# Kernel tuning notes

Measured on AMD Instinct MI355X. Metric: run time of the kernel, lower is better.

Reference implementation:

```python
import jax, jax.numpy as jnp
import numpy as np
import math

B, S, D = 8, 1024, 1024
NH, NKV, HD = 16, 8, 64
BLK_NUM, BLK_SIZE = 128, 8

def apply_rope(x, cos, sin):
    # x: (B,S,H,HD); cos/sin: (S, HD//2)
    x1 = x[..., 0::2]
    x2 = x[..., 1::2]
    c = cos[None, :, None, :]
    s = sin[None, :, None, :]
    r1 = x1 * c - x2 * s
    r2 = x1 * s + x2 * c
    out = jnp.stack([r1, r2], axis=-1).reshape(x.shape)
    return out

def setup_inputs() -> dict:
    key = jax.random.key(0)
    ks = jax.random.split(key, 7)
    x = jax.random.normal(ks[0], (B, S, D), dtype=jnp.float32)
    scale = 1.0 / math.sqrt(D)
    wq = jax.random.normal(ks[1], (D, NH * HD), dtype=jnp.float32) * scale
    wk = jax.random.normal(ks[2], (D, NKV * HD), dtype=jnp.float32) * scale
    wv = jax.random.normal(ks[3], (D, NKV * HD), dtype=jnp.float32) * scale
    wo = jax.random.normal(ks[4], (NH * HD, D), dtype=jnp.float32) * scale
    pos = jnp.arange(S, dtype=jnp.float32)
    inv_freq = 1.0 / (10000.0 ** (jnp.arange(0, HD, 2, dtype=jnp.float32) / HD))
    ang = pos[:, None] * inv_freq[None, :]
    freqs_cis_cos = jnp.cos(ang)
    freqs_cis_sin = jnp.sin(ang)
    return {"x": x, "wq": wq, "wk": wk, "wv": wv, "wo": wo,
            "freqs_cis_cos": freqs_cis_cos, "freqs_cis_sin": freqs_cis_sin,
            "start_pos": 0}

def reference(x, wq, wk, wv, wo, freqs_cis_cos, freqs_cis_sin, start_pos):
    q = (x @ wq).reshape(B, S, NH, HD)
    k = (x @ wk).reshape(B, S, NKV, HD)
    v = (x @ wv).reshape(B, S, NKV, HD)
    q = apply_rope(q, freqs_cis_cos, freqs_cis_sin)
    k = apply_rope(k, freqs_cis_cos, freqs_cis_sin)
    # GQA: repeat kv heads
    rep = NH // NKV
    k = jnp.repeat(k, rep, axis=2)  # (B,S,NH,HD)
    v = jnp.repeat(v, rep, axis=2)
    # block-causal mask: q in block i attends to kv blocks j <= i
    blk_id = jnp.arange(S) // BLK_SIZE
    mask = blk_id[:, None] >= blk_id[None, :]  # (S,S)
    scores = jnp.einsum('bqhd,bkhd->bhqk', q, k) / math.sqrt(HD)
    scores = jnp.where(mask[None, None], scores, -jnp.inf)
    attn = jax.nn.softmax(scores, axis=-1)
    out = jnp.einsum('bhqk,bkhd->bqhd', attn, v).reshape(B, S, NH * HD)
    return out @ wo
```

## Files before the change

### kernel.cpp

```cpp
#include <hip/hip_runtime.h>
#include <cstdint>
#include <math.h>

#define B_   8
#define S_   1024
#define D_   1024
#define NH_  16
#define NKV_ 8
#define HD_  64
#define M_   (B_*S_)

using bf16   = __bf16;
using bf16x4 = __attribute__((ext_vector_type(4))) __bf16;
using bf16x8 = __attribute__((ext_vector_type(8))) __bf16;
using f32x4  = __attribute__((ext_vector_type(4))) float;

__device__ __forceinline__ void gll16(const bf16* g, const bf16* l) {
    __builtin_amdgcn_global_load_lds(
        (const __attribute__((address_space(1))) unsigned int*)(uintptr_t)g,
        (__attribute__((address_space(3))) unsigned int*)(uintptr_t)l,
        16, 0, 0);
}

__device__ __forceinline__ void dsr128(bf16x8& d, const bf16* p) {
    asm volatile("ds_read_b128 %0, %1" : "=v"(d) : "v"((unsigned)(uintptr_t)p));
}
__device__ __forceinline__ void lgkm0() {
    asm volatile("s_waitcnt lgkmcnt(0)" ::: "memory");
    __builtin_amdgcn_sched_barrier(0);
}
__device__ __forceinline__ void vm_wait0()  { asm volatile("s_waitcnt vmcnt(0)"  ::: "memory"); }
__device__ __forceinline__ void vm_wait4()  { asm volatile("s_waitcnt vmcnt(4)"  ::: "memory"); }
__device__ __forceinline__ void vm_wait6()  { asm volatile("s_waitcnt vmcnt(6)"  ::: "memory"); }
__device__ __forceinline__ void vm_wait8()  { asm volatile("s_waitcnt vmcnt(8)"  ::: "memory"); }
__device__ __forceinline__ void bar()       { __builtin_amdgcn_s_barrier(); asm volatile("" ::: "memory"); }

__global__ void k_prep1(const float* __restrict__ x,
                        const float* __restrict__ wq, const float* __restrict__ wk,
                        const float* __restrict__ wv, const float* __restrict__ wo,
                        bf16* __restrict__ xb, bf16* __restrict__ wqkvT, bf16* __restrict__ woT) {
    __shared__ float tile[64 * 65];
    int bid = blockIdx.x;
    int t = threadIdx.x;
    if (bid < 8192) {
        int i = bid * 256 + t;
        float4 v = ((const float4*)x)[i];
        bf16x4 o = { (bf16)v.x, (bf16)v.y, (bf16)v.z, (bf16)v.w };
        ((bf16x4*)xb)[i] = o;
        return;
    }
    int b2 = bid - 8192;
    int bx = b2 % 48, by = b2 / 48;
    const int R = 1024;
    const float* in; bf16* out; int C, xo;
    if (bx < 16)      { in = wq; out = wqkvT;               C = 1024; xo = bx; }
    else if (bx < 24) { in = wk; out = wqkvT + 1024 * 1024; C = 512;  xo = bx - 16; }
    else if (bx < 32) { in = wv; out = wqkvT + 1536 * 1024; C = 512;  xo = bx - 24; }
    else              { in = wo; out = woT;                 C = 1024; xo = bx - 32; }
    int r0 = by * 64, c0 = xo * 64;
    #pragma unroll
    for (int it = 0; it < 16; ++it) {
        int idx = it * 256 + t;
        int r = idx >> 6, c = idx & 63;
        tile[r * 65 + c] = in[(size_t)(r0 + r) * C + c0 + c];
    }
    __syncthreads();
    #pragma unroll
    for (int it = 0; it < 16; ++it) {
        int idx = it * 256 + t;
        int c = idx >> 6, r = idx & 63;
        out[(size_t)(c0 + c) * R + r0 + r] = (bf16)tile[r * 65 + c];
    }
}

template <typename OutT, int NFR>
__global__ __launch_bounds__(256, 1) void k_gemmW(const bf16* __restrict__ A,
                                                  const bf16* __restrict__ Bt,
                                                  OutT* __restrict__ C, int M, int N, int K) {
    constexpr int BN = NFR * 32;
    __shared__ __align__(16) bf16 aL3[3 * 256 * 32];
    __shared__ __align__(16) bf16 bL3[3 * BN * 32];
    const int t    = threadIdx.x;
    const int lane = t & 63;
    const int w    = t >> 6;
    const int quad = lane >> 4;
    const int l16  = lane & 15;
    const int wr   = w >> 1;
    const int wc   = w & 1;

    int bid = blockIdx.y * gridDim.x + blockIdx.x;
    int cpx = (gridDim.x * gridDim.y) >> 3;
    int sw  = (bid & 7) * cpx + (bid >> 3);
    int bx  = sw % gridDim.x, by = sw / gridDim.x;
    const int m0 = by * 256;
    const int n0 = bx * BN;

    f32x4 acc[8][NFR] = {};

    auto stage = [&](int kb, int sb) {
        const int k0 = kb << 5;
        #pragma unroll
        for (int it = 0; it < 4; ++it) {
            int u = it * 256 + t;
            int r = u >> 2, c = u & 3;
            int cg = c ^ ((r & 3) ^ ((r >> 2) & 3));
            gll16(A + (size_t)(m0 + r) * K + k0 + cg * 8, aL3 + sb * (256 * 32) + u * 8);
        }
        #pragma unroll
        for (int it = 0; it < BN / 64; ++it) {
            int u = it * 256 + t;
            int r = u >> 2, c = u & 3;
            int cg = c ^ ((r & 3) ^ ((r >> 2) & 3));
            gll16(Bt + (size_t)(n0 + r) * K + k0 + cg * 8, bL3 + sb * (BN * 32) + u * 8);
        }
    };

    const int NT = K >> 5;

    stage(0, 0);
    stage(1, 1);

    int cur = 0;
    for (int T = 0; T < NT; ++T) {
        if (T + 1 < NT) { if constexpr (NFR == 8) vm_wait8(); else vm_wait6(); }
        else vm_wait0();
        bar();

        const bf16* aT = aL3 + cur * (256 * 32);
        const bf16* bT = bL3 + cur * (BN * 32);
        bf16x8 af[8], bf[NFR];
        #pragma unroll
        for (int mi = 0; mi < 8; ++mi) {
            int row = wr * 128 + mi * 16 + l16;
            int ch  = quad ^ ((row & 3) ^ ((row >> 2) & 3));
            af[mi] = *(const bf16x8*)&aT[row * 32 + ch * 8];
        }
        #pragma unroll
        for (int ni = 0; ni < NFR; ++ni) {
            int row = wc * (NFR * 16) + ni * 16 + l16;
            int ch  = quad ^ ((row & 3) ^ ((row >> 2) & 3));
            bf[ni] = *(const bf16x8*)&bT[row * 32 + ch * 8];
        }

        int stg = cur + 2; if (stg >= 3) stg -= 3;
        if (T + 2 < NT) stage(T + 2, stg);

        #pragma unroll
        for (int mi = 0; mi < 8; ++mi)
            #pragma unroll
            for (int ni = 0; ni < NFR; ++ni)
                acc[mi][ni] = __builtin_amdgcn_mfma_f32_16x16x32_bf16(af[mi], bf[ni], acc[mi][ni], 0, 0, 0);

        cur = (cur == 2) ? 0 : cur + 1;
    }

    #pragma unroll
    for (int mi = 0; mi < 8; ++mi)
        #pragma unroll
        for (int ni = 0; ni < NFR; ++ni)
            #pragma unroll
            for (int r = 0; r < 4; ++r) {
                int row = m0 + wr * 128 + mi * 16 + quad * 4 + r;
                int col = n0 + wc * (NFR * 16) + ni * 16 + l16;
                C[(size_t)row * N + col] = (OutT)acc[mi][ni][r];
            }
}

__global__ void k_prep2(const bf16* __restrict__ qkv, const float* __restrict__ cosg,
                        const float* __restrict__ sing, bf16* __restrict__ qd,
                        bf16* __restrict__ kd, bf16* __restrict__ vt) {
    __shared__ __align__(16) bf16 tile[64 * 72];
    int bid = blockIdx.x;
    int t = threadIdx.x;
    if (bid < 8192) {
        if (t < 192) {
            int token = bid;
            int b = token >> 10, s = token & 1023;
            int hh = t >> 3, i8 = t & 7;
            float4 c4 = *(const float4*)&cosg[s * 32 + i8 * 4];
            float4 s4 = *(const float4*)&sing[s * 32 + i8 * 4];
            int srcBase, dstBase;
            bf16* dst;
            float sf;
            if (hh < 16) {
                srcBase = token * 2048 + hh * 64;
                dstBase = ((b * NH_ + hh) * S_ + s) * 64;
                dst = qd;
                sf = 0.180336879f;
            } else {
                int h = hh - 16;
                srcBase = token * 2048 + 1024 + h * 64;
                dstBase = ((b * NKV_ + h) * S_ + s) * 64;
                dst = kd;
                sf = 1.0f;
            }
            bf16x8 v = *(const bf16x8*)&qkv[srcBase + i8 * 8];
            const float cc[4] = { c4.x, c4.y, c4.z, c4.w };
            const float ss[4] = { s4.x, s4.y, s4.z, s4.w };
            bf16x8 o;
            #pragma unroll
            for (int j = 0; j < 4; ++j) {
                float e  = (float)v[2 * j];
                float od = (float)v[2 * j + 1];
                o[2 * j]     = (bf16)(sf * (e * cc[j] - od * ss[j]));
                o[2 * j + 1] = (bf16)(sf * (e * ss[j] + od * cc[j]));
            }
            *(bf16x8*)&dst[dstBase + i8 * 8] = o;
        }
        return;
    }
    int b2 = bid - 8192;
    int st = b2 & 15;
    int h  = (b2 >> 4) & 7;
    int b  = b2 >> 7;
    int s0 = st * 64;
    #pragma unroll
    for (int it = 0; it < 2; ++it) {
        int ci = it * 256 + t;
        int r = ci >> 3, c = ci & 7;
        *(uint4*)&tile[r * 72 + c * 8] =
            *(const uint4*)&qkv[(size_t)(b * S_ + s0 + r) * 2048 + 1536 + h * 64 + c * 8];
    }
    __syncthreads();
    #pragma unroll
    for (int it = 0; it < 2; ++it) {
        int ci = it * 256 + t;
        int d = ci >> 3, sc = ci & 7;
        int g = sc >> 2, q4 = sc & 3;
        bf16x8 v;
        #pragma unroll
        for (int j = 0; j < 8; ++j) {
            int s_ext = g * 32 + q4 * 4 + (j & 3) + 16 * (j >> 2);
            v[j] = tile[s_ext * 72 + d];
        }
        *(bf16x8*)&vt[(size_t)((b * NKV_ + h) * 64 + d) * S_ + s0 + sc * 8] = v;
    }
}

__global__ __launch_bounds__(256, 4) void k_attn(const bf16* __restrict__ q, const bf16* __restrict__ k,
                                                 const bf16* __restrict__ vt, bf16* __restrict__ out) {
    __shared__ __align__(16) bf16 kt[2 * 64 * 64];
    __shared__ __align__(16) bf16 vtt[2 * 64 * 64];
    int bid = blockIdx.x;
    int qt = 15 - (bid >> 7);
    int combo = bid & 127;
    int b = combo >> 4, h = combo & 15;
    int hkv = h >> 1;
    int t = threadIdx.x;
    int w = t >> 6, lane = t & 63, quad = lane >> 4, l16 = lane & 15;

    const bf16* qh = q + (size_t)(b * NH_ + h) * S_ * 64;
    int qw = qt * 64 + w * 16;
    const bf16* qb = qh + (size_t)(qw + l16) * 64;
    bf16x8 qf0 = *(const bf16x8*)(qb + quad * 8);
    bf16x8 qf1 = *(const bf16x8*)(qb + 32 + quad * 8);

    const bf16* kg = k  + (size_t)(b * NKV_ + hkv) * S_ * 64;
    const bf16* vg = vt + (size_t)(b * NKV_ + hkv) * 64 * S_;

    const int sr0 = t >> 3;
    const int cs  = t & 7;

    auto stage = [&](int u, int buf) {
        int k0 = u * 64;
        #pragma unroll
        for (int it = 0; it < 2; ++it) {
            int r  = sr0 + it * 32;
            int cg = cs ^ (r & 7);
            int ci = it * 256 + t;
            gll16(kg + (size_t)(k0 + r) * 64 + cg * 8, kt  + buf * 4096 + ci * 8);
            gll16(vg + (size_t)r * S_ + k0 + cg * 8,   vtt + buf * 4096 + ci * 8);
        }
    };

    const bf16 one = (bf16)1.0f;
    const bf16x8 vones = { one, one, one, one, one, one, one, one };

    f32x4 o[4] = {};
    f32x4 ol = {};
    const int klim = ((qw + l16) & ~7) + 8;

    auto unit = [&](const bf16* ktb, const bf16* vtb, int k0, bool diag) {
        bf16x8 af[8];
        #pragma unroll
        for (int kk = 0; kk < 2; ++kk)
            #pragma unroll
            for (int f = 0; f < 4; ++f) {
                int row = f * 16 + l16;
                int ch  = (kk * 4 + quad) ^ (row & 7);
                dsr128(af[kk * 4 + f], &ktb[row * 64 + ch * 8]);
            }
        lgkm0();
        f32x4 sc[4] = {};
        __builtin_amdgcn_s_setprio(1);
        #pragma unroll
        for (int kk = 0; kk < 2; ++kk)
            #pragma unroll
            for (int f = 0; f < 4; ++f)
                sc[f] = __builtin_amdgcn_mfma_f32_16x16x32_bf16(af[kk * 4 + f], kk ? qf1 : qf0, sc[f], 0, 0, 0);
        __builtin_amdgcn_s_setprio(0);

        bf16x8 vbf[8];
        #pragma unroll
        for (int dc = 0; dc < 4; ++dc)
            #pragma unroll
            for (int kk = 0; kk < 2; ++kk) {
                int row = dc * 16 + l16;
                int ch  = (kk * 4 + quad) ^ (row & 7);
                dsr128(vbf[dc * 2 + kk], &vtb[row * 64 + ch * 8]);
            }

        float p[4][4];
        #pragma unroll
        for (int f = 0; f < 4; ++f)
            #pragma unroll
            for (int r = 0; r < 4; ++r) {
                float pv = __builtin_amdgcn_exp2f(sc[f][r]);
                if (diag && (k0 + f * 16 + quad * 4 + r >= klim)) pv = 0.f;
                p[f][r] = pv;
            }
        bf16x8 pa0, pa1;
        #pragma unroll
        for (int j = 0; j < 4; ++j) {
            pa0[j]     = (bf16)p[0][j];
            pa0[j + 4] = (bf16)p[1][j];
            pa1[j]     = (bf16)p[2][j];
            pa1[j + 4] = (bf16)p[3][j];
        }
        ol = __builtin_amdgcn_mfma_f32_16x16x32_bf16(pa0, vones, ol, 0, 0, 0);
        ol = __builtin_amdgcn_mfma_f32_16x16x32_bf16(pa1, vones, ol, 0, 0, 0);

        lgkm0();
        __builtin_amdgcn_s_setprio(1);
        #pragma unroll
        for (int dc = 0; dc < 4; ++dc)
            #pragma unroll
            for (int kk = 0; kk < 2; ++kk)
                o[dc] = __builtin_amdgcn_mfma_f32_16x16x32_bf16(kk ? pa1 : pa0, vbf[dc * 2 + kk], o[dc], 0, 0, 0);
        __builtin_amdgcn_s_setprio(0);
    };

    const int NU = qt + 1;
    stage(0, 0);
    asm volatile("" :: "v"(qf0), "v"(qf1));

    int u = 0;
    for (; u + 2 <= NU; u += 2) {
        bar();
        stage(u + 1, 1);
        vm_wait4();
        bar();
        unit(kt, vtt, u * 64, false);
        bar();
        bool hn = (u + 2 < NU);
        if (hn) { stage(u + 2, 0); vm_wait4(); } else vm_wait0();
        bar();
        unit(kt + 4096, vtt + 4096, (u + 1) * 64, (u + 1) == NU - 1);
    }
    if (u < NU) {
        bar();
        vm_wait0();
        bar();
        unit(kt, vtt, u * 64, true);
    }

    #pragma unroll
    for (int r = 0; r < 4; ++r) {
        float invl = 1.0f / ol[r];
        #pragma unroll
        for (int dc = 0; dc < 4; ++dc) {
            int row = qw + quad * 4 + r;
            int col = h * 64 + dc * 16 + l16;
            out[(size_t)(b * S_ + row) * 1024 + col] = (bf16)(o[dc][r] * invl);
        }
    }
}

extern "C" void kernel_launch(void* const* d_in, const int* in_sizes, int n_in,
                              void* d_out, int out_size, void* d_ws, size_t ws_size,
                              hipStream_t stream) {
    const float* x  = (const float*)d_in[0];
    const float* wq = (const float*)d_in[1];
    const float* wk = (const float*)d_in[2];
    const float* wv = (const float*)d_in[3];
    const float* wo = (const float*)d_in[4];
    const float* fc = (const float*)d_in[5];
    const float* fs = (const float*)d_in[6];
    (void)in_sizes; (void)n_in; (void)out_size; (void)ws_size;

    char* ws = (char*)d_ws;
    bf16* xb    = (bf16*)(ws);
    bf16* wqkvT = (bf16*)(ws + (16u << 20));
    bf16* woT   = (bf16*)(ws + (20u << 20));
    bf16* qkvb  = (bf16*)(ws + (22u << 20));
    bf16* kb    = (bf16*)(ws + (54u << 20));
    bf16* vtb   = (bf16*)(ws + (62u << 20));
    bf16* qb    = xb;
    bf16* attnb = qkvb;

    k_prep1<<<dim3(8960), dim3(256), 0, stream>>>(x, wq, wk, wv, wo, xb, wqkvT, woT);

    k_gemmW<bf16, 8><<<dim3(8, 32), dim3(256), 0, stream>>>(xb, wqkvT, qkvb, M_, 2048, 1024);

    k_prep2<<<dim3(9216), dim3(256), 0, stream>>>(qkvb, fc, fs, qb, kb, vtb);

    k_attn<<<dim3(2048), dim3(256), 0, stream>>>(qb, kb, vtb, attnb);

    k_gemmW<float, 4><<<dim3(8, 32), dim3(256), 0, stream>>>(attnb, woT, (float*)d_out, M_, 1024, 1024);
}
```

Baseline: 204.6 us.

## Replace wide GEMM with 128x128 double-buffered tile kernel at two blocks per CU

After: 190.9 us. -6.7%, faster.

```diff
diff --git a/kernel.cpp b/kernel.cpp
--- a/kernel.cpp
+++ b/kernel.cpp
@@ -31,7 +31,6 @@
 }
 __device__ __forceinline__ void vm_wait0()  { asm volatile("s_waitcnt vmcnt(0)"  ::: "memory"); }
 __device__ __forceinline__ void vm_wait4()  { asm volatile("s_waitcnt vmcnt(4)"  ::: "memory"); }
-__device__ __forceinline__ void vm_wait6()  { asm volatile("s_waitcnt vmcnt(6)"  ::: "memory"); }
 __device__ __forceinline__ void vm_wait8()  { asm volatile("s_waitcnt vmcnt(8)"  ::: "memory"); }
 __device__ __forceinline__ void bar()       { __builtin_amdgcn_s_barrier(); asm volatile("" ::: "memory"); }
 
@@ -73,13 +72,12 @@
     }
 }
 
-template <typename OutT, int NFR>
-__global__ __launch_bounds__(256, 1) void k_gemmW(const bf16* __restrict__ A,
-                                                  const bf16* __restrict__ Bt,
-                                                  OutT* __restrict__ C, int M, int N, int K) {
-    constexpr int BN = NFR * 32;
-    __shared__ __align__(16) bf16 aL3[3 * 256 * 32];
-    __shared__ __align__(16) bf16 bL3[3 * BN * 32];
+template <typename OutT>
+__global__ __launch_bounds__(256, 2) void k_gemm128(const bf16* __restrict__ A,
+                                                    const bf16* __restrict__ Bt,
+                                                    OutT* __restrict__ C, int M, int N, int K) {
+    __shared__ __align__(16) bf16 aL2[2 * 128 * 64];
+    __shared__ __align__(16) bf16 bL2[2 * 128 * 64];
     const int t    = threadIdx.x;
     const int lane = t & 63;
     const int w    = t >> 6;
@@ -92,76 +90,77 @@
     int cpx = (gridDim.x * gridDim.y) >> 3;
     int sw  = (bid & 7) * cpx + (bid >> 3);
     int bx  = sw % gridDim.x, by = sw / gridDim.x;
-    const int m0 = by * 256;
-    const int n0 = bx * BN;
-
-    f32x4 acc[8][NFR] = {};
+    const int m0 = by * 128;
+    const int n0 = bx * 128;
+
+    f32x4 acc[4][4] = {};
 
     auto stage = [&](int kb, int sb) {
-        const int k0 = kb << 5;
+        const int k0 = kb << 6;
         #pragma unroll
         for (int it = 0; it < 4; ++it) {
-            int u = it * 256 + t;
-            int r = u >> 2, c = u & 3;
-            int cg = c ^ ((r & 3) ^ ((r >> 2) & 3));
-            gll16(A + (size_t)(m0 + r) * K + k0 + cg * 8, aL3 + sb * (256 * 32) + u * 8);
-        }
-        #pragma unroll
-        for (int it = 0; it < BN / 64; ++it) {
-            int u = it * 256 + t;
-            int r = u >> 2, c = u & 3;
-            int cg = c ^ ((r & 3) ^ ((r >> 2) & 3));
-            gll16(Bt + (size_t)(n0 + r) * K + k0 + cg * 8, bL3 + sb * (BN * 32) + u * 8);
+            int ci = it * 256 + t;
+            int r = ci >> 3, c = ci & 7;
+            int cg = c ^ (r & 7);
+            gll16(A + (size_t)(m0 + r) * K + k0 + cg * 8, aL2 + sb * 8192 + ci * 8);
+        }
+        #pragma unroll
+        for (int it = 0; it < 4; ++it) {
+            int ci = it * 256 + t;
+            int r = ci >> 3, c = ci & 7;
+            int cg = c ^ (r & 7);
+            gll16(Bt + (size_t)(n0 + r) * K + k0 + cg * 8, bL2 + sb * 8192 + ci * 8);
         }
     };
 
-    const int NT = K >> 5;
+    const int NT = K >> 6;
+
+    auto tileStep = [&](int T, int buf) {
+        if (T + 1 < NT) { stage(T + 1, buf ^ 1); vm_wait8(); }
+        else vm_wait0();
+        bar();
+        const bf16* aL = aL2 + buf * 8192;
+        const bf16* bL = bL2 + buf * 8192;
+        #pragma unroll
+        for (int kk = 0; kk < 2; ++kk) {
+            bf16x8 af[4], bfr[4];
+            #pragma unroll
+            for (int mi = 0; mi < 4; ++mi) {
+                int row = wr * 64 + mi * 16 + l16;
+                int ch  = (kk * 4 + quad) ^ (row & 7);
+                af[mi] = *(const bf16x8*)&aL[row * 64 + ch * 8];
+            }
+            #pragma unroll
+            for (int ni = 0; ni < 4; ++ni) {
+                int row = wc * 64 + ni * 16 + l16;
+                int ch  = (kk * 4 + quad) ^ (row & 7);
+                bfr[ni] = *(const bf16x8*)&bL[row * 64 + ch * 8];
+            }
+            __builtin_amdgcn_s_setprio(1);
+            #pragma unroll
+            for (int mi = 0; mi < 4; ++mi)
+                #pragma unroll
+                for (int ni = 0; ni < 4; ++ni)
+                    acc[mi][ni] = __builtin_amdgcn_mfma_f32_16x16x32_bf16(af[mi], bfr[ni], acc[mi][ni], 0, 0, 0);
+            __builtin_amdgcn_s_setprio(0);
+        }
+        bar();
+    };
 
     stage(0, 0);
-    stage(1, 1);
-
-    int cur = 0;
-    for (int T = 0; T < NT; ++T) {
-        if (T + 1 < NT) { if constexpr (NFR == 8) vm_wait8(); else vm_wait6(); }
-        else vm_wait0();
-        bar();
-
-        const bf16* aT = aL3 + cur * (256 * 32);
-        const bf16* bT = bL3 + cur * (BN * 32);
-        bf16x8 af[8], bf[NFR];
-        #pragma unroll
-        for (int mi = 0; mi < 8; ++mi) {
-            int row = wr * 128 + mi * 16 + l16;
-            int ch  = quad ^ ((row & 3) ^ ((row >> 2) & 3));
-            af[mi] = *(const bf16x8*)&aT[row * 32 + ch * 8];
-        }
-        #pragma unroll
-        for (int ni = 0; ni < NFR; ++ni) {
-            int row = wc * (NFR * 16) + ni * 16 + l16;
-            int ch  = quad ^ ((row & 3) ^ ((row >> 2) & 3));
-            bf[ni] = *(const bf16x8*)&bT[row * 32 + ch * 8];
-        }
-
-        int stg = cur + 2; if (stg >= 3) stg -= 3;
-        if (T + 2 < NT) stage(T + 2, stg);
-
-        #pragma unroll
-        for (int mi = 0; mi < 8; ++mi)
-            #pragma unroll
-            for (int ni = 0; ni < NFR; ++ni)
-                acc[mi][ni] = __builtin_amdgcn_mfma_f32_16x16x32_bf16(af[mi], bf[ni], acc[mi][ni], 0, 0, 0);
-
-        cur = (cur == 2) ? 0 : cur + 1;
-    }
-
-    #pragma unroll
-    for (int mi = 0; mi < 8; ++mi)
-        #pragma unroll
-        for (int ni = 0; ni < NFR; ++ni)
+    for (int T = 0; T < NT; T += 2) {
+        tileStep(T, 0);
+        tileStep(T + 1, 1);
+    }
+
+    #pragma unroll
+    for (int mi = 0; mi < 4; ++mi)
+        #pragma unroll
+        for (int ni = 0; ni < 4; ++ni)
             #pragma unroll
             for (int r = 0; r < 4; ++r) {
-                int row = m0 + wr * 128 + mi * 16 + quad * 4 + r;
-                int col = n0 + wc * (NFR * 16) + ni * 16 + l16;
+                int row = m0 + wr * 64 + mi * 16 + quad * 4 + r;
+                int col = n0 + wc * 64 + ni * 16 + l16;
                 C[(size_t)row * N + col] = (OutT)acc[mi][ni][r];
             }
 }
@@ -400,11 +399,11 @@
 
     k_prep1<<<dim3(8960), dim3(256), 0, stream>>>(x, wq, wk, wv, wo, xb, wqkvT, woT);
 
-    k_gemmW<bf16, 8><<<dim3(8, 32), dim3(256), 0, stream>>>(xb, wqkvT, qkvb, M_, 2048, 1024);
+    k_gemm128<bf16><<<dim3(16, 64), dim3(256), 0, stream>>>(xb, wqkvT, qkvb, M_, 2048, 1024);
 
     k_prep2<<<dim3(9216), dim3(256), 0, stream>>>(qkvb, fc, fs, qb, kb, vtb);
 
     k_attn<<<dim3(2048), dim3(256), 0, stream>>>(qb, kb, vtb, attnb);
 
-    k_gemmW<float, 4><<<dim3(8, 32), dim3(256), 0, stream>>>(attnb, woT, (float*)d_out, M_, 1024, 1024);
-}
+    k_gemm128<float><<<dim3(8, 64), dim3(256), 0, stream>>>(attnb, woT, (float*)d_out, M_, 1024, 1024);
+}
```
